# Kernel optimization log

Hardware: AMD Instinct MI355X
Metric: run time of the kernel (lower is better)

Reference implementation:

```python
import jax, jax.numpy as jnp
import numpy as np

H, D = 2, 64          # heads, hidden_dim per head
HD = H * D            # 128
N_NODES = 50000
N_EDGES = 800000
N_GRAPHS = 64
IN_CH, EDGE_DIM, N_CLASSES = 2, 1, 30


def _tconv(x, src, dst, Wq, bq, Wk, bk, Wv, bv, We, Ws, bs):
    """PyG TransformerConv (concat=True, root_weight=True, beta=False)."""
    n = x.shape[0]
    q = (x @ Wq + bq).reshape(n, H, D)
    k = (x @ Wk + bk).reshape(n, H, D)
    v = (x @ Wv + bv).reshape(n, H, D)
    # edge embedding (lin_edge has no bias in PyG)
    return _attend(q, k, v, x @ Ws + bs, src, dst, We, n)


def _attend(q, k, v, skip, src, dst, We_e, n):
    kj = k[src] + We_e            # [E,H,D]
    vj = v[src] + We_e
    logits = (q[dst] * kj).sum(-1) / jnp.sqrt(jnp.asarray(D, q.dtype))  # [E,H]
    m = jax.ops.segment_max(logits, dst, num_segments=n)
    m = jnp.where(jnp.isfinite(m), m, jnp.zeros_like(m))
    ex = jnp.exp(logits - m[dst])
    denom = jax.ops.segment_sum(ex, dst, num_segments=n)
    alpha = ex / (denom[dst] + 1e-16)                                   # segment softmax
    agg = jax.ops.segment_sum(alpha[..., None] * vj, dst, num_segments=n)
    return agg.reshape(n, HD) + skip


def _forward(x, edge_index, edge_attr, batch,
             l0_Wq, l0_bq, l0_Wk, l0_bk, l0_Wv, l0_bv, l0_We, l0_Ws, l0_bs,
             l1_Wq, l1_bq, l1_Wk, l1_bk, l1_Wv, l1_bv, l1_We, l1_Ws, l1_bs,
             cW1, cb1, cW2, cb2):
    src, dst = edge_index[0], edge_index[1]
    e0 = (edge_attr @ l0_We).reshape(-1, H, D)
    e1 = (edge_attr @ l1_We).reshape(-1, H, D)
    n = x.shape[0]

    h = _attend((x @ l0_Wq + l0_bq).reshape(n, H, D),
                (x @ l0_Wk + l0_bk).reshape(n, H, D),
                (x @ l0_Wv + l0_bv).reshape(n, H, D),
                x @ l0_Ws + l0_bs, src, dst, e0, n)
    h = jax.nn.relu(h)
    h = _attend((h @ l1_Wq + l1_bq).reshape(n, H, D),
                (h @ l1_Wk + l1_bk).reshape(n, H, D),
                (h @ l1_Wv + l1_bv).reshape(n, H, D),
                h @ l1_Ws + l1_bs, src, dst, e1, n)
    h = jax.nn.relu(h)

    # global_mean_pool over graphs
    sums = jax.ops.segment_sum(h, batch, num_segments=N_GRAPHS)
    cnt = jax.ops.segment_sum(jnp.ones((n,), h.dtype), batch, num_segments=N_GRAPHS)
    g = sums / jnp.maximum(cnt, 1.0)[:, None]                           # [G, 128]

    return jax.nn.relu(g @ cW1 + cb1) @ cW2 + cb2                       # [G, 30]


def setup_inputs() -> dict:
    key = jax.random.key(0)
    ks = jax.random.split(key, 40)
    it = iter(ks)

    def lin(k, fan_in, fan_out):
        s = 1.0 / np.sqrt(fan_in)
        return jax.random.uniform(k, (fan_in, fan_out), jnp.float32, -s, s)

    inp = {
        'x': jax.random.normal(next(it), (N_NODES, IN_CH), jnp.float32),
        'edge_index': jax.random.randint(next(it), (2, N_EDGES), 0, N_NODES),
        'edge_attr': jax.random.normal(next(it), (N_EDGES, EDGE_DIM), jnp.float32),
        'batch': jnp.sort(jax.random.randint(next(it), (N_NODES,), 0, N_GRAPHS)),
    }
    for li, cin in (('l0', IN_CH), ('l1', HD)):
        for nm in ('Wq', 'Wk', 'Wv'):
            inp[f'{li}_{nm}'] = lin(next(it), cin, HD)
            inp[f'{li}_{nm.replace("W", "b")}'] = jax.random.uniform(
                next(it), (HD,), jnp.float32, -1 / np.sqrt(cin), 1 / np.sqrt(cin))
        inp[f'{li}_We'] = lin(next(it), EDGE_DIM, HD)
        inp[f'{li}_Ws'] = lin(next(it), cin, HD)
        inp[f'{li}_bs'] = jax.random.uniform(next(it), (HD,), jnp.float32,
                                             -1 / np.sqrt(cin), 1 / np.sqrt(cin))
    inp['cW1'] = lin(next(it), HD, 128)
    inp['cb1'] = jax.random.uniform(next(it), (128,), jnp.float32, -1 / np.sqrt(HD), 1 / np.sqrt(HD))
    inp['cW2'] = lin(next(it), 128, N_CLASSES)
    inp['cb2'] = jax.random.uniform(next(it), (N_CLASSES,), jnp.float32, -1 / np.sqrt(128), 1 / np.sqrt(128))
    return inp


def reference(x, edge_index, edge_attr, batch,
              l0_Wq, l0_bq, l0_Wk, l0_bk, l0_Wv, l0_bv, l0_We, l0_Ws, l0_bs,
              l1_Wq, l1_bq, l1_Wk, l1_bk, l1_Wv, l1_bv, l1_We, l1_Ws, l1_bs,
              cW1, cb1, cW2, cb2):
    return _forward(x, edge_index, edge_attr, batch,
                    l0_Wq, l0_bq, l0_Wk, l0_bk, l0_Wv, l0_bv, l0_We, l0_Ws, l0_bs,
                    l1_Wq, l1_bq, l1_Wk, l1_bk, l1_Wv, l1_bv, l1_We, l1_Ws, l1_bs,
                    cW1, cb1, cW2, cb2)
```

## Files before the change

### kernel.cpp

```cpp
#include <hip/hip_runtime.h>
#include <hip/hip_fp16.h>
#include <cstdint>
#include <cstddef>

#define HD 128

typedef short bf16x8 __attribute__((ext_vector_type(8)));
typedef float f32x4 __attribute__((ext_vector_type(4)));
typedef _Float16 h2f __attribute__((ext_vector_type(2)));

__device__ __forceinline__ h2f bits_to_h2(int v) {
    union { int i; h2f h; } u; u.i = v; return u.h;
}

#if __has_builtin(__builtin_amdgcn_fdot2)
#define DOT2(a, b) __builtin_amdgcn_fdot2((a), (b), 0.f, false)
#else
#define DOT2(a, b) fmaf((float)(a).x, (float)(b).x, (float)(a).y * (float)(b).y)
#endif

__device__ __forceinline__ unsigned short f2bf(float f) {
    unsigned int u = __float_as_uint(f);
    u += 0x7fff + ((u >> 16) & 1);
    return (unsigned short)(u >> 16);
}
__device__ __forceinline__ float bf2f(unsigned short h) {
    return __uint_as_float(((unsigned int)h) << 16);
}

template<int CTRL>
__device__ __forceinline__ float dpp_add(float x) {
    int y = __builtin_amdgcn_update_dpp(0, __float_as_int(x), CTRL, 0xF, 0xF, true);
    return x + __int_as_float(y);
}
__device__ __forceinline__ float half_reduce(float x) {
    x = dpp_add<0xB1>(x);
    x = dpp_add<0x4E>(x);
    x = dpp_add<0x124>(x);
    x = dpp_add<0x128>(x);
    x += __shfl_xor(x, 16, 64);
    return x;
}
__device__ __forceinline__ float wave_reduce(float x) {
    x = half_reduce(x);
    x += __shfl_xor(x, 32, 64);
    return x;
}

__device__ __forceinline__ void edge_pair(
    float& m, float& s, float& Sea, float2& acc, float cqwe, h2f q,
    int2 rawA, float aA, int2 rawB, float aB)
{
    h2f kA = bits_to_h2(rawA.x), vA = bits_to_h2(rawA.y);
    h2f kB = bits_to_h2(rawB.x), vB = bits_to_h2(rawB.y);
    float lA = fmaf(aA, cqwe, half_reduce(DOT2(q, kA)));
    float lB = fmaf(aB, cqwe, half_reduce(DOT2(q, kB)));
    float nm = fmaxf(fmaxf(m, lA), lB);
    float sc = __expf(m - nm);
    float eA = __expf(lA - nm);
    float eB = __expf(lB - nm);
    s   = fmaf(s, sc, eA + eB);
    Sea = fmaf(Sea, sc, fmaf(eA, aA, eB * aB));
    acc.x = fmaf(acc.x, sc, fmaf(eA, (float)vA.x, eB * (float)vB.x));
    acc.y = fmaf(acc.y, sc, fmaf(eA, (float)vA.y, eB * (float)vB.y));
    m = nm;
}
__device__ __forceinline__ void edge_single(
    float& m, float& s, float& Sea, float2& acc, float cqwe, h2f q,
    int2 rawA, float aA)
{
    h2f kA = bits_to_h2(rawA.x), vA = bits_to_h2(rawA.y);
    float lg = fmaf(aA, cqwe, half_reduce(DOT2(q, kA)));
    float nm = fmaxf(m, lg);
    float sc = __expf(m - nm);
    float ex = __expf(lg - nm);
    s   = fmaf(s, sc, ex);
    Sea = fmaf(Sea, sc, ex * aA);
    acc.x = fmaf(acc.x, sc, ex * (float)vA.x);
    acc.y = fmaf(acc.y, sc, ex * (float)vA.y);
    m = nm;
}

__global__ __launch_bounds__(256) void hist_kernel(
    const int* __restrict__ dst, int* __restrict__ cnt, int E)
{
    int e = blockIdx.x * 256 + threadIdx.x;
    if (e < E) atomicAdd(&cnt[dst[e]], 1);
}

__global__ __launch_bounds__(256) void scanA_kernel(
    const int* __restrict__ cnt, int* __restrict__ row_ptr,
    int* __restrict__ bsum, int n)
{
    __shared__ int sdata[256];
    int t = threadIdx.x;
    int base = blockIdx.x * 512 + 2 * t;
    int a = (base < n) ? cnt[base] : 0;
    int b = (base + 1 < n) ? cnt[base + 1] : 0;
    int local = a + b;
    sdata[t] = local;
    __syncthreads();
    #pragma unroll
    for (int off = 1; off < 256; off <<= 1) {
        int val = (t >= off) ? sdata[t - off] : 0;
        __syncthreads();
        sdata[t] += val;
        __syncthreads();
    }
    int excl = sdata[t] - local;
    if (base < n)     row_ptr[base] = excl;
    if (base + 1 < n) row_ptr[base + 1] = excl + a;
    if (t == 255) bsum[blockIdx.x] = sdata[255];
}

__global__ __launch_bounds__(256) void scanB_kernel(
    const int* __restrict__ bsum, int* __restrict__ boff, int B)
{
    __shared__ int sdata[256];
    int t = threadIdx.x;
    int local = (t < B) ? bsum[t] : 0;
    sdata[t] = local;
    __syncthreads();
    #pragma unroll
    for (int off = 1; off < 256; off <<= 1) {
        int val = (t >= off) ? sdata[t - off] : 0;
        __syncthreads();
        sdata[t] += val;
        __syncthreads();
    }
    if (t < B) boff[t] = sdata[t] - local;
}

__global__ __launch_bounds__(256) void scanC_kernel(
    int* __restrict__ row_ptr, int* __restrict__ cursor,
    const int* __restrict__ boff, int n, int E)
{
    int t = threadIdx.x;
    int base = blockIdx.x * 512 + 2 * t;
    int off = boff[blockIdx.x];
    if (base + 1 < n) {
        int2 v = *(int2*)&row_ptr[base];
        v.x += off; v.y += off;
        *(int2*)&row_ptr[base] = v;
        *(int2*)&cursor[base]  = v;
    } else if (base < n) {
        int v = row_ptr[base] + off;
        row_ptr[base] = v; cursor[base] = v;
    }
    if (blockIdx.x == 0 && t == 0) row_ptr[n] = E;
}

__global__ __launch_bounds__(256) void scatter_kernel(
    const int* __restrict__ dst, const int* __restrict__ src,
    const float* __restrict__ eattr, int* __restrict__ cursor,
    int2* __restrict__ epack, int E)
{
    int e = blockIdx.x * 256 + threadIdx.x;
    if (e < E) {
        int pos = atomicAdd(&cursor[dst[e]], 1);
        epack[pos] = make_int2(src[e], __float_as_int(eattr[e]));
    }
}

__global__ __launch_bounds__(128) void coef0_kernel(
    const float* __restrict__ Wq, const float* __restrict__ bq,
    const float* __restrict__ Wk, const float* __restrict__ bk,
    const float* __restrict__ We, float* __restrict__ coef)
{
    int w = threadIdx.x >> 6, l = threadIdx.x & 63;
    int j = w * 64 + l;
    float q0 = Wq[j], q1 = Wq[HD + j], qb = bq[j];
    float kv[4] = {Wk[j], Wk[HD + j], bk[j], We[j]};
    #pragma unroll
    for (int t = 0; t < 4; ++t) {
        float m0 = wave_reduce(kv[t] * q0);
        float m1 = wave_reduce(kv[t] * q1);
        float m2 = wave_reduce(kv[t] * qb);
        if (l == 0) {
            coef[w * 12 + t * 3 + 0] = m0 * 0.125f;
            coef[w * 12 + t * 3 + 1] = m1 * 0.125f;
            coef[w * 12 + t * 3 + 2] = m2 * 0.125f;
        }
    }
}

__global__ __launch_bounds__(256) void attn0a_kernel(
    const float* __restrict__ x, const float* __restrict__ coef,
    const int2* __restrict__ epack, const int* __restrict__ row_ptr,
    float4* __restrict__ S, int n)
{
    int i = blockIdx.x * 256 + threadIdx.x;
    if (i >= n) return;
    float C[24];
    #pragma unroll
    for (int t = 0; t < 24; ++t) C[t] = coef[t];
    float x0 = x[2 * i], x1 = x[2 * i + 1];
    float c0A = fmaf(x1, C[1],  fmaf(x0, C[0],  C[2]));
    float c1A = fmaf(x1, C[4],  fmaf(x0, C[3],  C[5]));
    float cbA = fmaf(x1, C[7],  fmaf(x0, C[6],  C[8]));
    float cwA = fmaf(x1, C[10], fmaf(x0, C[9],  C[11]));
    float c0B = fmaf(x1, C[13], fmaf(x0, C[12], C[14]));
    float c1B = fmaf(x1, C[16], fmaf(x0, C[15], C[17]));
    float cbB = fmaf(x1, C[19], fmaf(x0, C[18], C[20]));
    float cwB = fmaf(x1, C[22], fmaf(x0, C[21], C[23]));

    int p0 = row_ptr[i], p1 = row_ptr[i + 1];
    float mA = -INFINITY, sA = 0.f, SxA = 0.f, SyA = 0.f, SeA = 0.f;
    float mB = -INFINITY, sB = 0.f, SxB = 0.f, SyB = 0.f, SeB = 0.f;

    int2 epn = (p0 < p1) ? epack[p0] : make_int2(0, 0);
    for (int p = p0; p < p1; ++p) {
        int2 ep = epn;
        if (p + 1 < p1) epn = epack[p + 1];
        float ea = __int_as_float(ep.y);
        float2 xs = *(const float2*)&x[2 * ep.x];
        float lgA = fmaf(ea, cwA, fmaf(xs.y, c1A, fmaf(xs.x, c0A, cbA)));
        float lgB = fmaf(ea, cwB, fmaf(xs.y, c1B, fmaf(xs.x, c0B, cbB)));
        {
            float nm = fmaxf(mA, lgA);
            float sc = __expf(mA - nm);
            float ex = __expf(lgA - nm);
            sA  = fmaf(sA,  sc, ex);
            SxA = fmaf(SxA, sc, ex * xs.x);
            SyA = fmaf(SyA, sc, ex * xs.y);
            SeA = fmaf(SeA, sc, ex * ea);
            mA = nm;
        }
        {
            float nm = fmaxf(mB, lgB);
            float sc = __expf(mB - nm);
            float ex = __expf(lgB - nm);
            sB  = fmaf(sB,  sc, ex);
            SxB = fmaf(SxB, sc, ex * xs.x);
            SyB = fmaf(SyB, sc, ex * xs.y);
            SeB = fmaf(SeB, sc, ex * ea);
            mB = nm;
        }
    }
    S[(size_t)i * 2]     = make_float4(sA, SxA, SyA, SeA);
    S[(size_t)i * 2 + 1] = make_float4(sB, SxB, SyB, SeB);
}

__global__ __launch_bounds__(256) void attn_kernel(
    const __half* __restrict__ qh, const __half* __restrict__ kvh,
    const __half* __restrict__ sh, const float* __restrict__ We,
    const int2* __restrict__ epack, const int* __restrict__ row_ptr,
    __half2* __restrict__ outh, int n)
{
    int i = blockIdx.x * 4 + (threadIdx.x >> 6);
    if (i >= n) return;
    int l = threadIdx.x & 63;
    const int2* kv8 = (const int2*)kvh;
    const int* qraw = (const int*)qh;
    const __half2* sh2 = (const __half2*)sh;
    h2f q = bits_to_h2(qraw[(size_t)i * 64 + l]);
    float2 we = *(const float2*)&We[2 * l];
    float cqwe = half_reduce(fmaf((float)q.x, we.x, (float)q.y * we.y));
    int p0 = __builtin_amdgcn_readfirstlane(row_ptr[i]);
    int p1 = __builtin_amdgcn_readfirstlane(row_ptr[i + 1]);

    float m = -INFINITY, s = 0.f, Sea = 0.f;
    float2 acc = make_float2(0.f, 0.f);

    int2 kv0 = {}, kv1 = {}, kv2 = {}, kv3 = {};
    float ea0 = 0.f, ea1 = 0.f, ea2 = 0.f, ea3 = 0.f;

#define LD1(t, idx) do { if ((idx) < p1) { int2 ep_ = epack[idx]; \
    ea##t = __int_as_float(ep_.y); kv##t = kv8[(size_t)ep_.x * 64 + l]; } } while (0)

    LD1(0, p0); LD1(1, p0 + 1); LD1(2, p0 + 2); LD1(3, p0 + 3);

    int p = p0;
    for (; p + 3 < p1; p += 4) {
        int2 c0 = kv0, c1 = kv1, c2 = kv2, c3 = kv3;
        float a0 = ea0, a1 = ea1, a2 = ea2, a3 = ea3;
        LD1(0, p + 4); LD1(1, p + 5); LD1(2, p + 6); LD1(3, p + 7);
        edge_pair(m, s, Sea, acc, cqwe, q, c0, a0, c1, a1);
        edge_pair(m, s, Sea, acc, cqwe, q, c2, a2, c3, a3);
    }
    int rem = p1 - p;
    if (rem >= 2) edge_pair(m, s, Sea, acc, cqwe, q, kv0, ea0, kv1, ea1);
    if (rem == 1)      edge_single(m, s, Sea, acc, cqwe, q, kv0, ea0);
    else if (rem == 3) edge_single(m, s, Sea, acc, cqwe, q, kv2, ea2);

    float inv = 1.f / (s + 1e-16f);
    float2 skp = __half22float2(sh2[(size_t)i * 64 + l]);
    float rx = fmaxf(fmaf(fmaf(Sea, we.x, acc.x), inv, skp.x), 0.f);
    float ry = fmaxf(fmaf(fmaf(Sea, we.y, acc.y), inv, skp.y), 0.f);
    outh[(size_t)i * 64 + l] = __floats2half2_rn(rx, ry);
}

__global__ __launch_bounds__(256) void pack_kernel(
    const float* __restrict__ Wq, const float* __restrict__ Wk,
    const float* __restrict__ Wv, const float* __restrict__ Ws,
    const float* __restrict__ bq, const float* __restrict__ bk,
    const float* __restrict__ bv, const float* __restrict__ bs,
    unsigned short* __restrict__ Wph, unsigned short* __restrict__ Wpl,
    float* __restrict__ bias_cat)
{
    int id = blockIdx.x * 256 + threadIdx.x;
    if (id < 65536) {
        int j = id & 7, lane = (id >> 3) & 63, ks = (id >> 9) & 3, gnt = id >> 11;
        int k = ks * 32 + (lane >> 4) * 8 + j;
        int ncol = gnt * 16 + (lane & 15);
        int mat = ncol >> 7, d = ncol & 127;
        const float* W = (mat == 0) ? Wq : (mat == 1) ? Wk : (mat == 2) ? Wv : Ws;
        float w = W[k * HD + d];
        unsigned short hi = f2bf(w);
        Wph[id] = hi;
        Wpl[id] = f2bf(w - bf2f(hi));
    }
    if (id < 512) {
        int mat = id >> 7, d = id & 127;
        const float* b = (mat == 0) ? bq : (mat == 1) ? bk : (mat == 2) ? bv : bs;
        bias_cat[id] = b[d];
    }
}

__global__ __launch_bounds__(256) void lin1_mfma(
    const float* __restrict__ x, const float4* __restrict__ S0,
    const float* __restrict__ l0Wv, const float* __restrict__ l0bv,
    const float* __restrict__ l0We,
    const float* __restrict__ l0Ws, const float* __restrict__ l0bs,
    const unsigned short* __restrict__ Wph, const unsigned short* __restrict__ Wpl,
    const float* __restrict__ bias_cat,
    __half* __restrict__ qh, __half* __restrict__ kvh, __half* __restrict__ sh,
    int n)
{
    __shared__ float As[128 * 128];
    int tid = threadIdx.x;
    int row0 = blockIdx.x * 128;
    int yb = blockIdx.y;

    {
        int c4 = tid & 31;
        int c0 = c4 * 4;
        int rb = tid >> 5;
        int hh = c4 >> 4;
        float4 wv0 = *(const float4*)&l0Wv[c0];
        float4 wv1 = *(const float4*)&l0Wv[HD + c0];
        float4 bv4 = *(const float4*)&l0bv[c0];
        float4 we4 = *(const float4*)&l0We[c0];
        float4 ws0 = *(const float4*)&l0Ws[c0];
        float4 ws1 = *(const float4*)&l0Ws[HD + c0];
        float4 bs4 = *(const float4*)&l0bs[c0];
        #pragma unroll
        for (int it = 0; it < 16; ++it) {
            int r = it * 8 + rb;
            float4 av = make_float4(0.f, 0.f, 0.f, 0.f);
            if (row0 + r < n) {
                float2 xr = *(const float2*)&x[2 * (size_t)(row0 + r)];
                float4 Sv = S0[(size_t)(row0 + r) * 2 + hh];
                float inv = 1.f / (Sv.x + 1e-16f);
                float n0 = fmaf(wv0.x, Sv.y, fmaf(wv1.x, Sv.z, fmaf(bv4.x, Sv.x, we4.x * Sv.w)));
                float n1 = fmaf(wv0.y, Sv.y, fmaf(wv1.y, Sv.z, fmaf(bv4.y, Sv.x, we4.y * Sv.w)));
                float n2 = fmaf(wv0.z, Sv.y, fmaf(wv1.z, Sv.z, fmaf(bv4.z, Sv.x, we4.z * Sv.w)));
                float n3 = fmaf(wv0.w, Sv.y, fmaf(wv1.w, Sv.z, fmaf(bv4.w, Sv.x, we4.w * Sv.w)));
                av.x = fmaxf(fmaf(n0, inv, fmaf(xr.y, ws1.x, fmaf(xr.x, ws0.x, bs4.x))), 0.f);
                av.y = fmaxf(fmaf(n1, inv, fmaf(xr.y, ws1.y, fmaf(xr.x, ws0.y, bs4.y))), 0.f);
                av.z = fmaxf(fmaf(n2, inv, fmaf(xr.y, ws1.z, fmaf(xr.x, ws0.z, bs4.z))), 0.f);
                av.w = fmaxf(fmaf(n3, inv, fmaf(xr.y, ws1.w, fmaf(xr.x, ws0.w, bs4.w))), 0.f);
            }
            int sl = c4 ^ (r & 7);
            *(float4*)&As[r * 128 + sl * 4] = av;
        }
    }
    __syncthreads();

    int wave = tid >> 6, lane = tid & 63;
    int m = lane & 15, quad = lane >> 4;

    bf16x8 ah[2][4], al[2][4];
    #pragma unroll
    for (int sub = 0; sub < 2; ++sub) {
        int r = wave * 32 + sub * 16 + m;
        const float* base = &As[r * 128];
        int sw = r & 7;
        #pragma unroll
        for (int ks = 0; ks < 4; ++ks) {
            int i40 = (ks * 8 + quad * 2) ^ sw;
            int i41 = (ks * 8 + quad * 2 + 1) ^ sw;
            float4 x0 = *(const float4*)&base[i40 * 4];
            float4 x1 = *(const float4*)&base[i41 * 4];
            float v[8] = {x0.x, x0.y, x0.z, x0.w, x1.x, x1.y, x1.z, x1.w};
            #pragma unroll
            for (int j = 0; j < 8; ++j) {
                unsigned short hi = f2bf(v[j]);
                ah[sub][ks][j] = (short)hi;
                al[sub][ks][j] = (short)f2bf(v[j] - bf2f(hi));
            }
        }
    }
    __syncthreads();

    const bf16x8* PH = (const bf16x8*)Wph;
    const bf16x8* PL = (const bf16x8*)Wpl;
    __half2* qh2 = (__half2*)qh;
    __half2* sh2 = (__half2*)sh;
    __half*  kvS = (__half*)As;

    #define GNT_OF(nt) ((yb == 0) ? (((nt) < 8) ? (nt) : (nt) + 16) : (nt) + 8)

    bf16x8 bhA[4], blA[4], bhB[4], blB[4];
    {
        int g0 = GNT_OF(0);
        #pragma unroll
        for (int ks = 0; ks < 4; ++ks) {
            bhA[ks] = PH[(g0 * 4 + ks) * 64 + lane];
            blA[ks] = PL[(g0 * 4 + ks) * 64 + lane];
        }
    }

    for (int nt = 0; nt < 16; ++nt) {
        int gnt = GNT_OF(nt);
        if (nt + 1 < 16) {
            int g2 = GNT_OF(nt + 1);
            #pragma unroll
            for (int ks = 0; ks < 4; ++ks) {
                bhB[ks] = PH[(g2 * 4 + ks) * 64 + lane];
                blB[ks] = PL[(g2 * 4 + ks) * 64 + lane];
            }
        }
        f32x4 acc0 = {0.f, 0.f, 0.f, 0.f};
        f32x4 acc1 = {0.f, 0.f, 0.f, 0.f};
        #pragma unroll
        for (int ks = 0; ks < 4; ++ks) {
            acc0 = __builtin_amdgcn_mfma_f32_16x16x32_bf16(ah[0][ks], bhA[ks], acc0, 0, 0, 0);
            acc1 = __builtin_amdgcn_mfma_f32_16x16x32_bf16(ah[1][ks], bhA[ks], acc1, 0, 0, 0);
            acc0 = __builtin_amdgcn_mfma_f32_16x16x32_bf16(ah[0][ks], blA[ks], acc0, 0, 0, 0);
            acc1 = __builtin_amdgcn_mfma_f32_16x16x32_bf16(ah[1][ks], blA[ks], acc1, 0, 0, 0);
            acc0 = __builtin_amdgcn_mfma_f32_16x16x32_bf16(al[0][ks], bhA[ks], acc0, 0, 0, 0);
            acc1 = __builtin_amdgcn_mfma_f32_16x16x32_bf16(al[1][ks], bhA[ks], acc1, 0, 0, 0);
        }
        int ocol = gnt * 16 + m;
        int d = ocol & 127;
        float bias = bias_cat[ocol];
        if (yb == 0) {
            bool isq = (gnt < 8);
            __half2* dst = isq ? qh2 : sh2;
            float osc = isq ? 0.125f : 1.0f;
            bool evenl = (m & 1) == 0;
            #pragma unroll
            for (int sub = 0; sub < 2; ++sub) {
                f32x4 acc = sub ? acc1 : acc0;
                #pragma unroll
                for (int reg = 0; reg < 4; ++reg) {
                    int orow = row0 + wave * 32 + sub * 16 + quad * 4 + reg;
                    float val = (acc[reg] + bias) * osc;
                    float other = __shfl_xor(val, 1, 64);
                    if (orow < n && evenl)
                        dst[(size_t)orow * 64 + (d >> 1)] = __floats2half2_rn(val, other);
                }
            }
        } else {
            int slot = 4 * (d >> 1) + (d & 1) + ((gnt >= 16) ? 2 : 0);
            #pragma unroll
            for (int sub = 0; sub < 2; ++sub) {
                f32x4 acc = sub ? acc1 : acc0;
                #pragma unroll
                for (int reg = 0; reg < 4; ++reg) {
                    int row_l = wave * 32 + sub * 16 + quad * 4 + reg;
                    kvS[row_l * 256 + slot] = __float2half(acc[reg] + bias);
                }
            }
        }
        #pragma unroll
        for (int ks = 0; ks < 4; ++ks) { bhA[ks] = bhB[ks]; blA[ks] = blB[ks]; }
    }

    if (yb == 1) {
        __syncthreads();
        const float4* kvS4 = (const float4*)kvS;
        float4* kvh4 = (float4*)kvh;
        #pragma unroll
        for (int it = 0; it < 16; ++it) {
            int idx = it * 256 + tid;
            int row = idx >> 5, c4 = idx & 31;
            if (row0 + row < n)
                kvh4[(size_t)(row0 + row) * 32 + c4] = kvS4[row * 32 + c4];
        }
    }
    #undef GNT_OF
}

__global__ __launch_bounds__(128) void pool_kernel(
    const __half* __restrict__ h, const int* __restrict__ batch,
    float* __restrict__ gsums, float* __restrict__ gcnt, int n)
{
    __shared__ int sb[64];
    int i0 = blockIdx.x * 64;
    int d = threadIdx.x;
    int iend = i0 + 64; if (iend > n) iend = n;
    int csize = iend - i0;
    if (d < csize) sb[d] = batch[i0 + d];
    __syncthreads();
    if (csize <= 0) return;
    float local = 0.f;
    int cur = sb[0];
    int runc = 0;
    for (int i = i0; i < iend; ++i) {
        int g = sb[i - i0];
        if (g != cur) {
            atomicAdd(&gsums[(size_t)cur * HD + d], local);
            if (d == 0) atomicAdd(&gcnt[cur], (float)runc);
            local = 0.f; runc = 0; cur = g;
        }
        local += __half2float(h[(size_t)i * HD + d]);
        runc++;
    }
    atomicAdd(&gsums[(size_t)cur * HD + d], local);
    if (d == 0) atomicAdd(&gcnt[cur], (float)runc);
}

__global__ __launch_bounds__(128) void cls_kernel(
    const float* __restrict__ gsums, const float* __restrict__ gcnt,
    const float* __restrict__ cW1, const float* __restrict__ cb1,
    const float* __restrict__ cW2, const float* __restrict__ cb2,
    float* __restrict__ out)
{
    __shared__ float g[128];
    __shared__ float t[128];
    int gi = blockIdx.x, j = threadIdx.x;
    float c = fmaxf(gcnt[gi], 1.0f);
    g[j] = gsums[(size_t)gi * HD + j] / c;
    __syncthreads();
    float a = cb1[j];
    for (int k = 0; k < 128; ++k) a = fmaf(g[k], cW1[k * 128 + j], a);
    t[j] = fmaxf(a, 0.f);
    __syncthreads();
    if (j < 30) {
        float a2 = cb2[j];
        for (int k = 0; k < 128; ++k) a2 = fmaf(t[k], cW2[k * 30 + j], a2);
        out[gi * 30 + j] = a2;
    }
}

extern "C" void kernel_launch(void* const* d_in, const int* in_sizes, int n_in,
                              void* d_out, int out_size, void* d_ws, size_t ws_size,
                              hipStream_t stream)
{
    const float* x     = (const float*)d_in[0];
    const int*   ei    = (const int*)d_in[1];
    const float* eattr = (const float*)d_in[2];
    const int*   batch = (const int*)d_in[3];
    const float* l0_Wq = (const float*)d_in[4];
    const float* l0_bq = (const float*)d_in[5];
    const float* l0_Wk = (const float*)d_in[6];
    const float* l0_bk = (const float*)d_in[7];
    const float* l0_Wv = (const float*)d_in[8];
    const float* l0_bv = (const float*)d_in[9];
    const float* l0_We = (const float*)d_in[10];
    const float* l0_Ws = (const float*)d_in[11];
    const float* l0_bs = (const float*)d_in[12];
    const float* l1_Wq = (const float*)d_in[13];
    const float* l1_bq = (const float*)d_in[14];
    const float* l1_Wk = (const float*)d_in[15];
    const float* l1_bk = (const float*)d_in[16];
    const float* l1_Wv = (const float*)d_in[17];
    const float* l1_bv = (const float*)d_in[18];
    const float* l1_We = (const float*)d_in[19];
    const float* l1_Ws = (const float*)d_in[20];
    const float* l1_bs = (const float*)d_in[21];
    const float* cW1   = (const float*)d_in[22];
    const float* cb1   = (const float*)d_in[23];
    const float* cW2   = (const float*)d_in[24];
    const float* cb2   = (const float*)d_in[25];

    int n = in_sizes[0] / 2;
    int E = in_sizes[2];
    int G = out_size / 30;
    int B = (n + 511) / 512;

    size_t nd = (size_t)n * HD;
    __half* h1    = (__half*)d_ws;
    __half* qh    = h1 + nd;
    __half* sh    = qh + nd;
    __half* kvh   = sh + nd;
    float* bias_cat = (float*)(kvh + (size_t)n * 256);
    unsigned short* Wph = (unsigned short*)(bias_cat + 512);
    unsigned short* Wpl = Wph + 65536;
    float* coef   = (float*)(Wpl + 65536);
    float4* S0    = (float4*)(coef + 32);
    int2* epack   = (int2*)(S0 + (size_t)n * 2);
    int* cnt      = (int*)(epack + E);
    int* row_ptr  = cnt + n;
    int* cursor   = row_ptr + n + 2;
    int* bsum     = cursor + n;
    int* boff     = bsum + 256;
    float* gsums  = (float*)(boff + 256);
    float* gcnt   = gsums + (size_t)G * HD;

    const int* srcI = ei;
    const int* dstI = ei + E;

    hipMemsetAsync(cnt, 0, (size_t)n * sizeof(int), stream);
    hipMemsetAsync(gsums, 0, ((size_t)G * HD + G) * sizeof(float), stream);

    hist_kernel<<<(E + 255) / 256, 256, 0, stream>>>(dstI, cnt, E);
    scanA_kernel<<<B, 256, 0, stream>>>(cnt, row_ptr, bsum, n);
    scanB_kernel<<<1, 256, 0, stream>>>(bsum, boff, B);
    scanC_kernel<<<B, 256, 0, stream>>>(row_ptr, cursor, boff, n, E);
    scatter_kernel<<<(E + 255) / 256, 256, 0, stream>>>(dstI, srcI, eattr, cursor, epack, E);

    pack_kernel<<<256, 256, 0, stream>>>(l1_Wq, l1_Wk, l1_Wv, l1_Ws,
                                         l1_bq, l1_bk, l1_bv, l1_bs,
                                         Wph, Wpl, bias_cat);
    coef0_kernel<<<1, 128, 0, stream>>>(l0_Wq, l0_bq, l0_Wk, l0_bk, l0_We, coef);

    attn0a_kernel<<<(n + 255) / 256, 256, 0, stream>>>(
        x, coef, epack, row_ptr, S0, n);

    lin1_mfma<<<dim3((n + 127) / 128, 2), 256, 0, stream>>>(
        x, S0, l0_Wv, l0_bv, l0_We, l0_Ws, l0_bs,
        Wph, Wpl, bias_cat, qh, kvh, sh, n);
    attn_kernel<<<(n + 3) / 4, 256, 0, stream>>>(
        qh, kvh, sh, l1_We, epack, row_ptr, (__half2*)h1, n);

    pool_kernel<<<(n + 63) / 64, 128, 0, stream>>>(h1, batch, gsums, gcnt, n);
    cls_kernel<<<G, 128, 0, stream>>>(gsums, gcnt, cW1, cb1, cW2, cb2, (float*)d_out);
}
```

Baseline: 356.3 us.

## Fuse mean-pool into attention via atomics and merge lin1 column halves into one block

The second-layer attention kernel now adds each node's ReLU output straight into per-graph sums with float atomics. This removes the h1 buffer write and the separate pool kernel. The classifier recovers per-graph node counts by binary search on the batch array, which assumes batch is sorted. The lin1 MFMA kernel drops its 2-way y-grid split, so each block computes all 32 column tiles and reuses the staged A tile, but only half as many blocks launch. The fused pooling sends every element of every node to the same 64x128 addresses, which risks heavy atomic contention.

```diff
diff --git a/kernel.cpp b/kernel.cpp
--- a/kernel.cpp
+++ b/kernel.cpp
@@ -245,7 +245,7 @@
     const __half* __restrict__ qh, const __half* __restrict__ kvh,
     const __half* __restrict__ sh, const float* __restrict__ We,
     const int2* __restrict__ epack, const int* __restrict__ row_ptr,
-    __half2* __restrict__ outh, int n)
+    const int* __restrict__ batch, float* __restrict__ gsums, int n)
 {
     int i = blockIdx.x * 4 + (threadIdx.x >> 6);
     if (i >= n) return;
@@ -287,7 +287,9 @@
     float2 skp = __half22float2(sh2[(size_t)i * 64 + l]);
     float rx = fmaxf(fmaf(fmaf(Sea, we.x, acc.x), inv, skp.x), 0.f);
     float ry = fmaxf(fmaf(fmaf(Sea, we.y, acc.y), inv, skp.y), 0.f);
-    outh[(size_t)i * 64 + l] = __floats2half2_rn(rx, ry);
+    int gi = __builtin_amdgcn_readfirstlane(batch[i]);
+    atomicAdd(&gsums[(size_t)gi * HD + 2 * l],     rx);
+    atomicAdd(&gsums[(size_t)gi * HD + 2 * l + 1], ry);
 }
 
 __global__ __launch_bounds__(256) void pack_kernel(
@@ -330,7 +332,6 @@
     __shared__ float As[128 * 128];
     int tid = threadIdx.x;
     int row0 = blockIdx.x * 128;
-    int yb = blockIdx.y;
 
     {
         int c4 = tid & 31;
@@ -399,26 +400,19 @@
     __half2* sh2 = (__half2*)sh;
     __half*  kvS = (__half*)As;
 
-    #define GNT_OF(nt) ((yb == 0) ? (((nt) < 8) ? (nt) : (nt) + 16) : (nt) + 8)
-
     bf16x8 bhA[4], blA[4], bhB[4], blB[4];
-    {
-        int g0 = GNT_OF(0);
-        #pragma unroll
-        for (int ks = 0; ks < 4; ++ks) {
-            bhA[ks] = PH[(g0 * 4 + ks) * 64 + lane];
-            blA[ks] = PL[(g0 * 4 + ks) * 64 + lane];
-        }
-    }
-
-    for (int nt = 0; nt < 16; ++nt) {
-        int gnt = GNT_OF(nt);
-        if (nt + 1 < 16) {
-            int g2 = GNT_OF(nt + 1);
+    #pragma unroll
+    for (int ks = 0; ks < 4; ++ks) {
+        bhA[ks] = PH[ks * 64 + lane];
+        blA[ks] = PL[ks * 64 + lane];
+    }
+
+    for (int gnt = 0; gnt < 32; ++gnt) {
+        if (gnt + 1 < 32) {
             #pragma unroll
             for (int ks = 0; ks < 4; ++ks) {
-                bhB[ks] = PH[(g2 * 4 + ks) * 64 + lane];
-                blB[ks] = PL[(g2 * 4 + ks) * 64 + lane];
+                bhB[ks] = PH[((gnt + 1) * 4 + ks) * 64 + lane];
+                blB[ks] = PL[((gnt + 1) * 4 + ks) * 64 + lane];
             }
         }
         f32x4 acc0 = {0.f, 0.f, 0.f, 0.f};
@@ -435,7 +429,8 @@
         int ocol = gnt * 16 + m;
         int d = ocol & 127;
         float bias = bias_cat[ocol];
-        if (yb == 0) {
+        bool iskv = (gnt >= 8) && (gnt < 24);
+        if (!iskv) {
             bool isq = (gnt < 8);
             __half2* dst = isq ? qh2 : sh2;
             float osc = isq ? 0.125f : 1.0f;
@@ -468,60 +463,33 @@
         for (int ks = 0; ks < 4; ++ks) { bhA[ks] = bhB[ks]; blA[ks] = blB[ks]; }
     }
 
-    if (yb == 1) {
-        __syncthreads();
-        const float4* kvS4 = (const float4*)kvS;
-        float4* kvh4 = (float4*)kvh;
-        #pragma unroll
-        for (int it = 0; it < 16; ++it) {
-            int idx = it * 256 + tid;
-            int row = idx >> 5, c4 = idx & 31;
-            if (row0 + row < n)
-                kvh4[(size_t)(row0 + row) * 32 + c4] = kvS4[row * 32 + c4];
-        }
-    }
-    #undef GNT_OF
-}
-
-__global__ __launch_bounds__(128) void pool_kernel(
-    const __half* __restrict__ h, const int* __restrict__ batch,
-    float* __restrict__ gsums, float* __restrict__ gcnt, int n)
-{
-    __shared__ int sb[64];
-    int i0 = blockIdx.x * 64;
-    int d = threadIdx.x;
-    int iend = i0 + 64; if (iend > n) iend = n;
-    int csize = iend - i0;
-    if (d < csize) sb[d] = batch[i0 + d];
-    __syncthreads();
-    if (csize <= 0) return;
-    float local = 0.f;
-    int cur = sb[0];
-    int runc = 0;
-    for (int i = i0; i < iend; ++i) {
-        int g = sb[i - i0];
-        if (g != cur) {
-            atomicAdd(&gsums[(size_t)cur * HD + d], local);
-            if (d == 0) atomicAdd(&gcnt[cur], (float)runc);
-            local = 0.f; runc = 0; cur = g;
-        }
-        local += __half2float(h[(size_t)i * HD + d]);
-        runc++;
-    }
-    atomicAdd(&gsums[(size_t)cur * HD + d], local);
-    if (d == 0) atomicAdd(&gcnt[cur], (float)runc);
+    __syncthreads();
+    const float4* kvS4 = (const float4*)kvS;
+    float4* kvh4 = (float4*)kvh;
+    #pragma unroll
+    for (int it = 0; it < 16; ++it) {
+        int idx = it * 256 + tid;
+        int row = idx >> 5, c4 = idx & 31;
+        if (row0 + row < n)
+            kvh4[(size_t)(row0 + row) * 32 + c4] = kvS4[row * 32 + c4];
+    }
 }
 
 __global__ __launch_bounds__(128) void cls_kernel(
-    const float* __restrict__ gsums, const float* __restrict__ gcnt,
+    const float* __restrict__ gsums, const int* __restrict__ batch,
     const float* __restrict__ cW1, const float* __restrict__ cb1,
     const float* __restrict__ cW2, const float* __restrict__ cb2,
-    float* __restrict__ out)
+    float* __restrict__ out, int n)
 {
     __shared__ float g[128];
     __shared__ float t[128];
     int gi = blockIdx.x, j = threadIdx.x;
-    float c = fmaxf(gcnt[gi], 1.0f);
+    int lo = 0, hi = n;
+    while (lo < hi) { int mid = (lo + hi) >> 1; if (batch[mid] < gi) lo = mid + 1; else hi = mid; }
+    int start = lo;
+    lo = start; hi = n;
+    while (lo < hi) { int mid = (lo + hi) >> 1; if (batch[mid] < gi + 1) lo = mid + 1; else hi = mid; }
+    float c = fmaxf((float)(lo - start), 1.0f);
     g[j] = gsums[(size_t)gi * HD + j] / c;
     __syncthreads();
     float a = cb1[j];
@@ -572,8 +540,7 @@
     int B = (n + 511) / 512;
 
     size_t nd = (size_t)n * HD;
-    __half* h1    = (__half*)d_ws;
-    __half* qh    = h1 + nd;
+    __half* qh    = (__half*)d_ws;
     __half* sh    = qh + nd;
     __half* kvh   = sh + nd;
     float* bias_cat = (float*)(kvh + (size_t)n * 256);
@@ -588,13 +555,12 @@
     int* bsum     = cursor + n;
     int* boff     = bsum + 256;
     float* gsums  = (float*)(boff + 256);
-    float* gcnt   = gsums + (size_t)G * HD;
 
     const int* srcI = ei;
     const int* dstI = ei + E;
 
     hipMemsetAsync(cnt, 0, (size_t)n * sizeof(int), stream);
-    hipMemsetAsync(gsums, 0, ((size_t)G * HD + G) * sizeof(float), stream);
+    hipMemsetAsync(gsums, 0, (size_t)G * HD * sizeof(float), stream);
 
     hist_kernel<<<(E + 255) / 256, 256, 0, stream>>>(dstI, cnt, E);
     scanA_kernel<<<B, 256, 0, stream>>>(cnt, row_ptr, bsum, n);
@@ -610,12 +576,12 @@
     attn0a_kernel<<<(n + 255) / 256, 256, 0, stream>>>(
         x, coef, epack, row_ptr, S0, n);
 
-    lin1_mfma<<<dim3((n + 127) / 128, 2), 256, 0, stream>>>(
+    lin1_mfma<<<(n + 127) / 128, 256, 0, stream>>>(
         x, S0, l0_Wv, l0_bv, l0_We, l0_Ws, l0_bs,
         Wph, Wpl, bias_cat, qh, kvh, sh, n);
     attn_kernel<<<(n + 3) / 4, 256, 0, stream>>>(
-        qh, kvh, sh, l1_We, epack, row_ptr, (__half2*)h1, n);
-
-    pool_kernel<<<(n + 63) / 64, 128, 0, stream>>>(h1, batch, gsums, gcnt, n);
-    cls_kernel<<<G, 128, 0, stream>>>(gsums, gcnt, cW1, cb1, cW2, cb2, (float*)d_out);
-}
+        qh, kvh, sh, l1_We, epack, row_ptr, batch, gsums, n);
+
+    cls_kernel<<<G, 128, 0, stream>>>(gsums, batch, cW1, cb1, cW2, cb2,
+                                      (float*)d_out, n);
+}
```

Measured after the change: 446.8 us. 25.4% more time.
